# Optimization experiments

Hardware: AMD Instinct MI355X
Metric: run time of the kernel (lower is better)

Reference implementation:

```python
import jax, jax.numpy as jnp
import numpy as np

B, S, D = 4, 2048, 768
H = 12
DH = D // H
NUM_WAY = 4
DFF = 4 * D  # FFN expansion scale=4
EPS = 1e-6


def setup_inputs() -> dict:
    key = jax.random.key(0)
    ks = jax.random.split(key, 20)
    s = 0.02
    inp = {
        "x": jax.random.normal(ks[0], (B, S, D), jnp.float32),
        "w": jax.random.randint(ks[1], (B, S), 0, NUM_WAY, jnp.int64),
        # LayerNorm 1
        "ln1_g": jnp.ones((D,), jnp.float32),
        "ln1_b": jnp.zeros((D,), jnp.float32),
        # Multi-head attention projections (input_dim=out_dim=D)
        "wq": jax.random.normal(ks[2], (D, D), jnp.float32) * s,
        "bq": jnp.zeros((D,), jnp.float32),
        "wk": jax.random.normal(ks[3], (D, D), jnp.float32) * s,
        "bk": jnp.zeros((D,), jnp.float32),
        "wv": jax.random.normal(ks[4], (D, D), jnp.float32) * s,
        "bv": jnp.zeros((D,), jnp.float32),
        "wo": jax.random.normal(ks[5], (D, D), jnp.float32) * s,
        "bo": jnp.zeros((D,), jnp.float32),
        # Way classifier
        "wcls": jax.random.normal(ks[6], (D, NUM_WAY), jnp.float32) * s,
        "bcls": jnp.zeros((NUM_WAY,), jnp.float32),
        # num_way stacked FFN experts: Linear(D,4D) -> ReLU -> Linear(4D,D)
        "w1": jax.random.normal(ks[7], (NUM_WAY, D, DFF), jnp.float32) * s,
        "b1": jnp.zeros((NUM_WAY, DFF), jnp.float32),
        "w2": jax.random.normal(ks[8], (NUM_WAY, DFF, D), jnp.float32) * s,
        "b2": jnp.zeros((NUM_WAY, D), jnp.float32),
    }
    return inp


def _layernorm(x, g, b):
    mu = jnp.mean(x, axis=-1, keepdims=True)
    var = jnp.mean(jnp.square(x - mu), axis=-1, keepdims=True)
    return (x - mu) * jax.lax.rsqrt(var + EPS) * g + b


def reference(x, w, ln1_g, ln1_b, wq, bq, wk, bk, wv, bv, wo, bo,
              wcls, bcls, w1, b1, w2, b2):
    # pre-LN
    xn = _layernorm(x, ln1_g, ln1_b)
    # multi-head self-attention (q = k = v = xn)
    q = (xn @ wq + bq).reshape(B, S, H, DH)
    k = (xn @ wk + bk).reshape(B, S, H, DH)
    v = (xn @ wv + bv).reshape(B, S, H, DH)
    scores = jnp.einsum('bqhd,bkhd->bhqk', q, k) / jnp.sqrt(jnp.float32(DH))
    attn = jax.nn.softmax(scores, axis=-1)
    ctx = jnp.einsum('bhqk,bkhd->bqhd', attn, v).reshape(B, S, D)
    ctx = ctx @ wo + bo
    # dropout is identity at inference; residual
    out = ctx + x
    # dense compute-all-experts FFN, then per-token select by routing id w
    # (mask-overwrite in original == one-hot select since masks partition)
    ffn_out = jnp.zeros_like(out)
    for ci in range(NUM_WAY):
        h = jax.nn.relu(out @ w1[ci] + b1[ci])        # [B,S,4D]
        fi = h @ w2[ci] + b2[ci]                      # [B,S,D]
        mask = (w == ci).astype(out.dtype)[..., None]  # [B,S,1]
        if ci == 0:
            # original initializes ffn_out with way-0 output everywhere;
            # later ways overwrite where w == ci, net = select expert w
            ffn_out = fi
        else:
            ffn_out = ffn_out * (1.0 - mask) + fi * mask
    way_logits = out @ wcls + bcls  # [B,S,NUM_WAY]
    return ffn_out, way_logits
```

## Files before the change

### kernel.cpp

```cpp
#include <hip/hip_runtime.h>
#include <cstdint>

typedef unsigned short u16;
typedef float f32x4 __attribute__((ext_vector_type(4)));
typedef __bf16 bf16x8 __attribute__((ext_vector_type(8)));

#define LOG2E 1.44269504088896340736f

__device__ __forceinline__ u16 f2bf(float f) {
    union { float f; unsigned u; } v; v.f = f;
    unsigned r = v.u + 0x7fffu + ((v.u >> 16) & 1u);
    return (u16)(r >> 16);
}

__device__ __forceinline__ unsigned cvt_pk_bf16(float lo, float hi) {
    unsigned r;
    asm("v_cvt_pk_bf16_f32 %0, %1, %2" : "=v"(r) : "v"(lo), "v"(hi));
    return r;
}

__device__ __forceinline__ f32x4 mfma16(bf16x8 a, bf16x8 b, f32x4 c) {
    return __builtin_amdgcn_mfma_f32_16x16x32_bf16(a, b, c, 0, 0, 0);
}

__device__ __forceinline__ void gload_lds16(const void* g, void* l) {
    __builtin_amdgcn_global_load_lds(
        (__attribute__((address_space(1))) unsigned int*)(g),
        (__attribute__((address_space(3))) unsigned int*)(l),
        16, 0, 0);
}

#define MB_TOK 8192
#define DM 768
#define HH 12
#define DHD 64
#define NWAY 4
#define DFF 3072
#define SEQ 2048
#define NBATCH 4

__global__ __launch_bounds__(256) void ln_kernel(
    const float* __restrict__ x, const float* __restrict__ g,
    const float* __restrict__ bb, u16* __restrict__ xn)
{
    int row = blockIdx.x, t = threadIdx.x;
    const float* xr = x + (size_t)row * DM;
    float v0 = xr[t], v1 = xr[t + 256], v2 = xr[t + 512];
    float s = v0 + v1 + v2;
    __shared__ float red[4];
    #pragma unroll
    for (int k = 1; k < 64; k <<= 1) s += __shfl_xor(s, k);
    if ((t & 63) == 0) red[t >> 6] = s;
    __syncthreads();
    float mu = (red[0] + red[1] + red[2] + red[3]) * (1.f / 768.f);
    float d0 = v0 - mu, d1 = v1 - mu, d2 = v2 - mu;
    float q = d0 * d0 + d1 * d1 + d2 * d2;
    #pragma unroll
    for (int k = 1; k < 64; k <<= 1) q += __shfl_xor(q, k);
    __syncthreads();
    if ((t & 63) == 0) red[t >> 6] = q;
    __syncthreads();
    float var = (red[0] + red[1] + red[2] + red[3]) * (1.f / 768.f);
    float rs = rsqrtf(var + 1e-6f);
    u16* xo = xn + (size_t)row * DM;
    xo[t]       = f2bf(d0 * rs * g[t]       + bb[t]);
    xo[t + 256] = f2bf(d1 * rs * g[t + 256] + bb[t + 256]);
    xo[t + 512] = f2bf(d2 * rs * g[t + 512] + bb[t + 512]);
}

__global__ __launch_bounds__(256) void transpose_bf16(
    const float* __restrict__ src, u16* __restrict__ dst, int K, int N)
{
    __shared__ float tl[32][33];
    size_t bofs = (size_t)blockIdx.z * K * N;
    src += bofs; dst += bofs;
    int n0 = blockIdx.x * 32, k0 = blockIdx.y * 32;
    int tx = threadIdx.x, ty = threadIdx.y;
    #pragma unroll
    for (int j = 0; j < 4; ++j)
        tl[ty + j * 8][tx] = src[(size_t)(k0 + ty + j * 8) * N + n0 + tx];
    __syncthreads();
    #pragma unroll
    for (int j = 0; j < 4; ++j)
        dst[(size_t)(n0 + ty + j * 8) * K + k0 + tx] = f2bf(tl[tx][ty + j * 8]);
}

__global__ __launch_bounds__(256) void vT_kernel(
    const u16* __restrict__ qkv, u16* __restrict__ vT)
{
    __shared__ u16 tl[32][33];
    int bh = blockIdx.z;
    int b = bh / HH, h = bh % HH;
    int key0 = blockIdx.x * 32;
    int d0 = blockIdx.y * 32;
    int tx = threadIdx.x, ty = threadIdx.y;
    const u16* src = qkv + ((size_t)b * SEQ + key0) * 2304 + 1536 + h * 64 + d0;
    #pragma unroll
    for (int j = 0; j < 4; ++j)
        tl[ty + j * 8][tx] = src[(size_t)(ty + j * 8) * 2304 + tx];
    __syncthreads();
    u16* dst = vT + ((size_t)bh * 64 + d0) * SEQ + key0;
    #pragma unroll
    for (int j = 0; j < 4; ++j)
        dst[(size_t)(ty + j * 8) * SEQ + tx] = tl[tx][ty + j * 8];
}

__global__ void concat_bias_kernel(const float* bq, const float* bk,
                                   const float* bv, float* bqkv)
{
    int i = blockIdx.x * 256 + threadIdx.x;
    if (i < 2304) bqkv[i] = i < 768 ? bq[i] : (i < 1536 ? bk[i - 768] : bv[i - 1536]);
}

__global__ void route_kernel(const int* __restrict__ wl,
                             int* __restrict__ perm, int* __restrict__ eoff,
                             int4* __restrict__ fmap)
{
    __shared__ int cnt[4], cur[4], off[5];
    int tid = threadIdx.x;
    if (tid < 4) cnt[tid] = 0;
    __syncthreads();
    for (int t = tid; t < MB_TOK; t += 256) atomicAdd(&cnt[wl[t] & 3], 1);
    __syncthreads();
    if (tid == 0) {
        off[0] = 0;
        for (int e = 0; e < 4; ++e) off[e + 1] = off[e] + cnt[e];
        int idx = 0;
        for (int e = 0; e < 4; ++e)
            for (int s = 0; s < cnt[e]; s += 128)
                fmap[idx++] = make_int4(e, off[e], s, cnt[e] - s);
        for (; idx < 68; ++idx) fmap[idx] = make_int4(-1, 0, 0, 0);
        for (int e = 0; e < 5; ++e) eoff[e] = off[e];
        for (int e = 0; e < 4; ++e) cur[e] = off[e];
    }
    __syncthreads();
    for (int t = tid; t < MB_TOK; t += 256) {
        int e = wl[t] & 3;
        int pos = atomicAdd(&cur[e], 1);
        perm[pos] = t;
    }
}

template<int MODE, bool RELU, bool RES, bool ST32, bool ST16>
__global__ __launch_bounds__(256, 2) void gemm_bt_kernel(
    const u16* __restrict__ A, const u16* __restrict__ Bt,
    const float* __restrict__ bias, const float* __restrict__ res,
    float* __restrict__ out32, u16* __restrict__ out16,
    int M, int N, int K, int ntn,
    const int* __restrict__ perm, const int4* __restrict__ fmap)
{
    __shared__ __attribute__((aligned(16))) u16 As[128 * 32];
    __shared__ __attribute__((aligned(16))) u16 Bs[128 * 32];
    int tid = threadIdx.x;
    int wv = tid >> 6, ln = tid & 63;
    int bt = blockIdx.x / ntn;
    int tn = (blockIdx.x % ntn) * 128;

    int seg = 0, ms = 0, mb = 128, tm = 0;
    if (MODE != 0) {
        int4 ent = fmap[bt];
        if (ent.x < 0) return;
        seg = ent.y; ms = ent.z; mb = ent.w; if (mb > 128) mb = 128;
        Bt += (size_t)ent.x * N * K;
        bias += ent.x * N;
    } else {
        tm = bt * 128;
    }

    f32x4 acc[4][4];
    #pragma unroll
    for (int i = 0; i < 4; ++i)
        #pragma unroll
        for (int j = 0; j < 4; ++j) acc[i][j] = f32x4{0.f, 0.f, 0.f, 0.f};

    int wr = wv >> 1, wc = wv & 1;
    int lr = ln & 15, hi = ln >> 4;
    int nk = K / 32;

    for (int kk = 0; kk < nk; ++kk) {
        int k0 = kk * 32;
        #pragma unroll
        for (int i = 0; i < 2; ++i) {
            int r = (wv * 2 + i) * 16 + (ln >> 2);
            int am = r < mb ? r : (mb - 1);
            size_t arow;
            if (MODE == 1)      arow = (size_t)perm[seg + ms + am];
            else if (MODE == 2) arow = (size_t)(seg + ms + am);
            else                arow = (size_t)(tm + r);
            gload_lds16(A + arow * K + k0 + (ln & 3) * 8, &As[(wv * 2 + i) * 512]);
        }
        #pragma unroll
        for (int i = 0; i < 2; ++i) {
            int r = (wv * 2 + i) * 16 + (ln >> 2);
            gload_lds16(Bt + (size_t)(tn + r) * K + k0 + (ln & 3) * 8,
                        &Bs[(wv * 2 + i) * 512]);
        }
        __syncthreads();
        bf16x8 a[4], b[4];
        #pragma unroll
        for (int m = 0; m < 4; ++m)
            a[m] = *(const bf16x8*)&As[(wr * 64 + m * 16 + lr) * 32 + hi * 8];
        #pragma unroll
        for (int n = 0; n < 4; ++n)
            b[n] = *(const bf16x8*)&Bs[(wc * 64 + n * 16 + lr) * 32 + hi * 8];
        #pragma unroll
        for (int m = 0; m < 4; ++m)
            #pragma unroll
            for (int n = 0; n < 4; ++n)
                acc[m][n] = mfma16(a[m], b[n], acc[m][n]);
        __syncthreads();
    }

    #pragma unroll
    for (int m = 0; m < 4; ++m) {
        int rb = wr * 64 + m * 16 + hi * 4;
        #pragma unroll
        for (int n = 0; n < 4; ++n) {
            int gcol = tn + wc * 64 + n * 16 + lr;
            float bvv = bias[gcol];
            #pragma unroll
            for (int i = 0; i < 4; ++i) {
                int rml = rb + i;
                float v = acc[m][n][i] + bvv;
                if (RELU) v = v > 0.f ? v : 0.f;
                if (MODE == 0) {
                    size_t grow = (size_t)(tm + rml);
                    if (RES) v += res[grow * N + gcol];
                    if (ST32) out32[grow * N + gcol] = v;
                    if (ST16) out16[grow * N + gcol] = f2bf(v);
                } else {
                    if (rml < mb) {
                        size_t orow = (MODE == 1) ? (size_t)(seg + ms + rml)
                                                  : (size_t)perm[seg + ms + rml];
                        if (ST32) out32[orow * N + gcol] = v;
                        if (ST16) out16[orow * N + gcol] = f2bf(v);
                    }
                }
            }
        }
    }
}

__global__ __launch_bounds__(256, 4) void attn_kernel(
    const u16* __restrict__ qkv, const u16* __restrict__ vT,
    u16* __restrict__ ctx)
{
    __shared__ __attribute__((aligned(16))) u16 Ks[64 * 64];
    __shared__ __attribute__((aligned(16))) u16 Vs[64 * 64];
    int tid = threadIdx.x;
    int wv = tid >> 6, ln = tid & 63;
    int lr = ln & 15, hi = ln >> 4;
    int bh = blockIdx.y;
    int b = bh / HH, h = bh % HH;
    int q0 = blockIdx.x * 64 + wv * 16;
    size_t qrow = (size_t)(b * SEQ + q0 + lr);
    const float C = 0.125f * LOG2E;

    bf16x8 qf[2];
    {
        const u16* qp = qkv + qrow * 2304 + h * 64 + hi * 8;
        qf[0] = *(const bf16x8*)qp;
        qf[1] = *(const bf16x8*)(qp + 32);
    }
    f32x4 o[4];
    #pragma unroll
    for (int i = 0; i < 4; ++i) o[i] = f32x4{0.f, 0.f, 0.f, 0.f};
    float m_run = -INFINITY, l_run = 0.f;

    const size_t kbase = (size_t)b * SEQ * 2304 + 768 + h * 64;
    const u16* vtb = vT + (size_t)bh * 64 * SEQ;
    int scol = (ln & 7) * 8;

    for (int kt = 0; kt < SEQ / 64; ++kt) {
        int key0 = kt * 64;
        #pragma unroll
        for (int i = 0; i < 2; ++i) {
            int r = wv * 16 + i * 8 + (ln >> 3);
            int csrc = scol ^ ((r & 7) * 8);
            gload_lds16(qkv + kbase + (size_t)(key0 + r) * 2304 + csrc,
                        &Ks[(wv * 2 + i) * 512]);
            gload_lds16(vtb + (size_t)r * SEQ + key0 + csrc,
                        &Vs[(wv * 2 + i) * 512]);
        }
        __syncthreads();

        f32x4 sf[4];
        #pragma unroll
        for (int f = 0; f < 4; ++f) {
            int key = f * 16 + lr;
            int sw = (key & 7) * 8;
            bf16x8 klo = *(const bf16x8*)&Ks[key * 64 + ((hi * 8) ^ sw)];
            bf16x8 khi = *(const bf16x8*)&Ks[key * 64 + ((32 + hi * 8) ^ sw)];
            f32x4 s = f32x4{0.f, 0.f, 0.f, 0.f};
            s = mfma16(klo, qf[0], s);
            s = mfma16(khi, qf[1], s);
            sf[f] = s;
        }

        float tmax = sf[0][0];
        #pragma unroll
        for (int f = 0; f < 4; ++f)
            #pragma unroll
            for (int i = 0; i < 4; ++i) tmax = fmaxf(tmax, sf[f][i]);
        tmax = fmaxf(tmax, __shfl_xor(tmax, 16));
        tmax = fmaxf(tmax, __shfl_xor(tmax, 32));

        if (!__all(tmax - m_run <= 64.f)) {
            float m_new = fmaxf(m_run, tmax);
            float corr = exp2f((m_run - m_new) * C);
            l_run *= corr;
            #pragma unroll
            for (int dg = 0; dg < 4; ++dg) {
                o[dg][0] *= corr; o[dg][1] *= corr;
                o[dg][2] *= corr; o[dg][3] *= corr;
            }
            m_run = m_new;
        }

        float c2 = -m_run * C;
        float p[4][4];
        float psum = 0.f;
        #pragma unroll
        for (int f = 0; f < 4; ++f)
            #pragma unroll
            for (int i = 0; i < 4; ++i) {
                p[f][i] = exp2f(fmaf(sf[f][i], C, c2));
                psum += p[f][i];
            }
        psum += __shfl_xor(psum, 16);
        psum += __shfl_xor(psum, 32);
        l_run += psum;

        #pragma unroll
        for (int kf = 0; kf < 2; ++kf) {
            union { bf16x8 v; unsigned u[4]; } pb;
            pb.u[0] = cvt_pk_bf16(p[2 * kf][0], p[2 * kf][1]);
            pb.u[1] = cvt_pk_bf16(p[2 * kf][2], p[2 * kf][3]);
            pb.u[2] = cvt_pk_bf16(p[2 * kf + 1][0], p[2 * kf + 1][1]);
            pb.u[3] = cvt_pk_bf16(p[2 * kf + 1][2], p[2 * kf + 1][3]);
            #pragma unroll
            for (int dg = 0; dg < 4; ++dg) {
                int d = dg * 16 + lr;
                int sw = (d & 7) * 16;
                const char* vb = (const char*)Vs + d * 128;
                union { bf16x8 v; uint2 u[2]; } va;
                va.u[0] = *(const uint2*)(const void*)(vb + ((kf * 64 + hi * 8) ^ sw));
                va.u[1] = *(const uint2*)(const void*)(vb + ((kf * 64 + hi * 8 + 32) ^ sw));
                o[dg] = mfma16(va.v, pb.v, o[dg]);
            }
        }
        __syncthreads();
    }

    float inv = 1.f / l_run;
    #pragma unroll
    for (int dg = 0; dg < 4; ++dg) {
        uint2 pk;
        pk.x = cvt_pk_bf16(o[dg][0] * inv, o[dg][1] * inv);
        pk.y = cvt_pk_bf16(o[dg][2] * inv, o[dg][3] * inv);
        *(uint2*)(void*)&ctx[qrow * DM + h * 64 + dg * 16 + hi * 4] = pk;
    }
}

__global__ __launch_bounds__(256) void cls_kernel(
    const float* __restrict__ outm, const float* __restrict__ wcls,
    const float* __restrict__ bcls, float* __restrict__ dst)
{
    int row = blockIdx.x, t = threadIdx.x;
    const float* xr = outm + (size_t)row * DM;
    float a0 = 0, a1 = 0, a2 = 0, a3 = 0;
    for (int j = t; j < DM; j += 256) {
        float xv = xr[j];
        float4 wv4 = *(const float4*)(const void*)(wcls + (size_t)j * 4);
        a0 += xv * wv4.x; a1 += xv * wv4.y; a2 += xv * wv4.z; a3 += xv * wv4.w;
    }
    #pragma unroll
    for (int k = 1; k < 64; k <<= 1) {
        a0 += __shfl_xor(a0, k); a1 += __shfl_xor(a1, k);
        a2 += __shfl_xor(a2, k); a3 += __shfl_xor(a3, k);
    }
    __shared__ float red[4][4];
    if ((t & 63) == 0) {
        int wid = t >> 6;
        red[wid][0] = a0; red[wid][1] = a1; red[wid][2] = a2; red[wid][3] = a3;
    }
    __syncthreads();
    if (t < 4)
        dst[(size_t)row * 4 + t] =
            red[0][t] + red[1][t] + red[2][t] + red[3][t] + bcls[t];
}

extern "C" void kernel_launch(void* const* d_in, const int* in_sizes, int n_in,
                              void* d_out, int out_size, void* d_ws, size_t ws_size,
                              hipStream_t stream) {
    const float* x      = (const float*)d_in[0];
    const int*   wl     = (const int*)d_in[1];
    const float* ln_g   = (const float*)d_in[2];
    const float* ln_b   = (const float*)d_in[3];
    const float* wq     = (const float*)d_in[4];
    const float* bq     = (const float*)d_in[5];
    const float* wk     = (const float*)d_in[6];
    const float* bk     = (const float*)d_in[7];
    const float* wvv    = (const float*)d_in[8];
    const float* bv     = (const float*)d_in[9];
    const float* wo     = (const float*)d_in[10];
    const float* bo     = (const float*)d_in[11];
    const float* wcls   = (const float*)d_in[12];
    const float* bcls   = (const float*)d_in[13];
    const float* w1     = (const float*)d_in[14];
    const float* b1     = (const float*)d_in[15];
    const float* w2     = (const float*)d_in[16];
    const float* b2     = (const float*)d_in[17];
    float* out = (float*)d_out;

    char* ws = (char*)d_ws;
    u16*   xn    = (u16*)  (ws + 0);
    u16*   qkv   = (u16*)  (ws + 12582912);
    u16*   hbuf  = (u16*)  (ws + 0);
    u16*   ctx   = (u16*)  (ws + 50331648);
    u16*   outb  = (u16*)  (ws + 62914560);
    u16*   wqkvt = (u16*)  (ws + 75497472);
    u16*   wot   = (u16*)  (ws + 79036416);
    u16*   w1t   = (u16*)  (ws + 80216064);
    u16*   w2t   = (u16*)  (ws + 99090432);
    float* bqkv  = (float*)(ws + 117964800);
    int*   perm  = (int*)  (ws + 117974016);
    int*   eoff  = (int*)  (ws + 118006784);
    int4*  fmap  = (int4*) (ws + 118006816);
    u16*   vT    = (u16*)  (ws + 118008064);
    float* outf  = out;

    route_kernel<<<1, 256, 0, stream>>>(wl, perm, eoff, fmap);
    concat_bias_kernel<<<9, 256, 0, stream>>>(bq, bk, bv, bqkv);
    dim3 tb(32, 8);
    transpose_bf16<<<dim3(24, 24, 1), tb, 0, stream>>>(wq,  wqkvt,             768, 768);
    transpose_bf16<<<dim3(24, 24, 1), tb, 0, stream>>>(wk,  wqkvt + 768 * 768, 768, 768);
    transpose_bf16<<<dim3(24, 24, 1), tb, 0, stream>>>(wvv, wqkvt + 2 * 768 * 768, 768, 768);
    transpose_bf16<<<dim3(24, 24, 1), tb, 0, stream>>>(wo,  wot, 768, 768);
    transpose_bf16<<<dim3(96, 24, 4), tb, 0, stream>>>(w1,  w1t, 768, 3072);
    transpose_bf16<<<dim3(24, 96, 4), tb, 0, stream>>>(w2,  w2t, 3072, 768);
    ln_kernel<<<MB_TOK, 256, 0, stream>>>(x, ln_g, ln_b, xn);

    gemm_bt_kernel<0, false, false, false, true><<<64 * 18, 256, 0, stream>>>(
        xn, wqkvt, bqkv, nullptr, nullptr, qkv, MB_TOK, 2304, 768, 18, nullptr, nullptr);

    vT_kernel<<<dim3(64, 2, 48), tb, 0, stream>>>(qkv, vT);

    attn_kernel<<<dim3(32, 48), 256, 0, stream>>>(qkv, vT, ctx);

    gemm_bt_kernel<0, false, true, true, true><<<64 * 6, 256, 0, stream>>>(
        ctx, wot, bo, x, outf, outb, MB_TOK, 768, 768, 6, nullptr, nullptr);

    cls_kernel<<<MB_TOK, 256, 0, stream>>>(outf, wcls, bcls, out + (size_t)MB_TOK * DM);

    gemm_bt_kernel<1, true, false, false, true><<<68 * 24, 256, 0, stream>>>(
        outb, w1t, b1, nullptr, nullptr, hbuf, MB_TOK, DFF, 768, 24, perm, fmap);

    gemm_bt_kernel<2, false, false, true, false><<<68 * 6, 256, 0, stream>>>(
        hbuf, w2t, b2, nullptr, out, nullptr, MB_TOK, 768, DFF, 6, perm, fmap);
}
```

Measured before the change: 410.5 us.

## Restructure attention to 32x32 MFMA tiles with double-buffered K/V and LDS-staged output

The attention kernel now gives each wave 32 query rows using 32x32x16 bf16 MFMAs instead of 16x16x32, so each block covers 128 queries. K/V tiles are double-buffered in LDS so the next tile's loads overlap the current tile's compute, which removes one barrier per iteration. exp2 is mapped directly to the hardware v_exp_f32, P fragments are rearranged with a cross-half lane shuffle, and the output is staged through LDS for coalesced 16-byte stores. The grid is flattened and remapped across heads and batches. The cost is more registers per thread and doubled LDS, which may lower occupancy.

```diff
diff --git a/kernel.cpp b/kernel.cpp
--- a/kernel.cpp
+++ b/kernel.cpp
@@ -3,6 +3,7 @@
 
 typedef unsigned short u16;
 typedef float f32x4 __attribute__((ext_vector_type(4)));
+typedef float f32x16 __attribute__((ext_vector_type(16)));
 typedef __bf16 bf16x8 __attribute__((ext_vector_type(8)));
 
 #define LOG2E 1.44269504088896340736f
@@ -19,8 +20,18 @@
     return r;
 }
 
+__device__ __forceinline__ float exp2_hw(float x) {
+    float r;
+    asm("v_exp_f32 %0, %1" : "=v"(r) : "v"(x));
+    return r;
+}
+
 __device__ __forceinline__ f32x4 mfma16(bf16x8 a, bf16x8 b, f32x4 c) {
     return __builtin_amdgcn_mfma_f32_16x16x32_bf16(a, b, c, 0, 0, 0);
+}
+
+__device__ __forceinline__ f32x16 mfma32(bf16x8 a, bf16x8 b, f32x16 c) {
+    return __builtin_amdgcn_mfma_f32_32x32x16_bf16(a, b, c, 0, 0, 0);
 }
 
 __device__ __forceinline__ void gload_lds16(const void* g, void* l) {
@@ -245,120 +256,140 @@
     const u16* __restrict__ qkv, const u16* __restrict__ vT,
     u16* __restrict__ ctx)
 {
-    __shared__ __attribute__((aligned(16))) u16 Ks[64 * 64];
-    __shared__ __attribute__((aligned(16))) u16 Vs[64 * 64];
+    __shared__ __attribute__((aligned(16))) u16 Ks[2][4096];
+    __shared__ __attribute__((aligned(16))) u16 Vs[2][4096];
     int tid = threadIdx.x;
     int wv = tid >> 6, ln = tid & 63;
-    int lr = ln & 15, hi = ln >> 4;
-    int bh = blockIdx.y;
+    int qv = ln & 31, hi = ln >> 5;
+    int bid = blockIdx.x;
+    int bh = (bid & 7) * 6 + ((bid >> 3) % 6);
+    int qt = (bid >> 3) / 6;
     int b = bh / HH, h = bh % HH;
-    int q0 = blockIdx.x * 64 + wv * 16;
-    size_t qrow = (size_t)(b * SEQ + q0 + lr);
+    int q0 = qt * 128 + wv * 32;
+    size_t qrowb = (size_t)(b * SEQ + q0);
     const float C = 0.125f * LOG2E;
 
-    bf16x8 qf[2];
+    bf16x8 qf[4];
     {
-        const u16* qp = qkv + qrow * 2304 + h * 64 + hi * 8;
-        qf[0] = *(const bf16x8*)qp;
-        qf[1] = *(const bf16x8*)(qp + 32);
-    }
-    f32x4 o[4];
-    #pragma unroll
-    for (int i = 0; i < 4; ++i) o[i] = f32x4{0.f, 0.f, 0.f, 0.f};
-    float m_run = -INFINITY, l_run = 0.f;
-
+        const u16* qp = qkv + (qrowb + qv) * 2304 + h * 64 + hi * 8;
+        #pragma unroll
+        for (int ds = 0; ds < 4; ++ds) qf[ds] = *(const bf16x8*)(qp + ds * 16);
+    }
+
+    int csrc = 8 * ((ln & 7) ^ (ln >> 3));
     const size_t kbase = (size_t)b * SEQ * 2304 + 768 + h * 64;
     const u16* vtb = vT + (size_t)bh * 64 * SEQ;
-    int scol = (ln & 7) * 8;
+    const u16* kp0 = qkv + kbase + (size_t)(wv * 16 + (ln >> 3)) * 2304 + csrc;
+    const u16* kp1 = kp0 + (size_t)8 * 2304;
+    const u16* vp0 = vtb + (size_t)(wv * 16 + (ln >> 3)) * SEQ + csrc;
+    const u16* vp1 = vp0 + (size_t)8 * SEQ;
+
+#define ATTN_STAGE(bf_, t_) do {                                          \
+    gload_lds16(kp0 + (size_t)(t_) * 64 * 2304, &Ks[bf_][(wv * 2) * 512]);\
+    gload_lds16(kp1 + (size_t)(t_) * 64 * 2304, &Ks[bf_][(wv * 2 + 1) * 512]);\
+    gload_lds16(vp0 + (size_t)(t_) * 64, &Vs[bf_][(wv * 2) * 512]);       \
+    gload_lds16(vp1 + (size_t)(t_) * 64, &Vs[bf_][(wv * 2 + 1) * 512]);   \
+} while (0)
+
+    f32x16 oacc[2];
+    #pragma unroll
+    for (int i = 0; i < 2; ++i)
+        #pragma unroll
+        for (int r = 0; r < 16; ++r) oacc[i][r] = 0.f;
+    float m_run = -INFINITY, l_run = 0.f;
+    int ksw = (qv & 7) * 8;
+
+    ATTN_STAGE(0, 0);
 
     for (int kt = 0; kt < SEQ / 64; ++kt) {
-        int key0 = kt * 64;
-        #pragma unroll
-        for (int i = 0; i < 2; ++i) {
-            int r = wv * 16 + i * 8 + (ln >> 3);
-            int csrc = scol ^ ((r & 7) * 8);
-            gload_lds16(qkv + kbase + (size_t)(key0 + r) * 2304 + csrc,
-                        &Ks[(wv * 2 + i) * 512]);
-            gload_lds16(vtb + (size_t)r * SEQ + key0 + csrc,
-                        &Vs[(wv * 2 + i) * 512]);
-        }
+        int bf = kt & 1;
         __syncthreads();
-
-        f32x4 sf[4];
-        #pragma unroll
-        for (int f = 0; f < 4; ++f) {
-            int key = f * 16 + lr;
-            int sw = (key & 7) * 8;
-            bf16x8 klo = *(const bf16x8*)&Ks[key * 64 + ((hi * 8) ^ sw)];
-            bf16x8 khi = *(const bf16x8*)&Ks[key * 64 + ((32 + hi * 8) ^ sw)];
-            f32x4 s = f32x4{0.f, 0.f, 0.f, 0.f};
-            s = mfma16(klo, qf[0], s);
-            s = mfma16(khi, qf[1], s);
-            sf[f] = s;
-        }
-
-        float tmax = sf[0][0];
-        #pragma unroll
-        for (int f = 0; f < 4; ++f)
-            #pragma unroll
-            for (int i = 0; i < 4; ++i) tmax = fmaxf(tmax, sf[f][i]);
-        tmax = fmaxf(tmax, __shfl_xor(tmax, 16));
+        if (kt + 1 < SEQ / 64) ATTN_STAGE(bf ^ 1, kt + 1);
+
+        f32x16 s0, s1;
+        #pragma unroll
+        for (int r = 0; r < 16; ++r) { s0[r] = 0.f; s1[r] = 0.f; }
+        #pragma unroll
+        for (int ds = 0; ds < 4; ++ds) {
+            bf16x8 ka0 = *(const bf16x8*)&Ks[bf][qv * 64 + ((ds * 16 + hi * 8) ^ ksw)];
+            bf16x8 ka1 = *(const bf16x8*)&Ks[bf][(32 + qv) * 64 + ((ds * 16 + hi * 8) ^ ksw)];
+            s0 = mfma32(ka0, qf[ds], s0);
+            s1 = mfma32(ka1, qf[ds], s1);
+        }
+
+        float tmax = s0[0];
+        #pragma unroll
+        for (int r = 1; r < 16; ++r) tmax = fmaxf(tmax, s0[r]);
+        #pragma unroll
+        for (int r = 0; r < 16; ++r) tmax = fmaxf(tmax, s1[r]);
         tmax = fmaxf(tmax, __shfl_xor(tmax, 32));
 
         if (!__all(tmax - m_run <= 64.f)) {
             float m_new = fmaxf(m_run, tmax);
-            float corr = exp2f((m_run - m_new) * C);
+            float corr = exp2_hw((m_run - m_new) * C);
             l_run *= corr;
             #pragma unroll
-            for (int dg = 0; dg < 4; ++dg) {
-                o[dg][0] *= corr; o[dg][1] *= corr;
-                o[dg][2] *= corr; o[dg][3] *= corr;
+            for (int i = 0; i < 2; ++i)
+                #pragma unroll
+                for (int r = 0; r < 16; ++r) oacc[i][r] *= corr;
+            m_run = m_new;
+        }
+        float c2 = -m_run * C;
+        float psum = 0.f;
+        #pragma unroll
+        for (int r = 0; r < 16; ++r) {
+            s0[r] = exp2_hw(fmaf(s0[r], C, c2)); psum += s0[r];
+            s1[r] = exp2_hw(fmaf(s1[r], C, c2)); psum += s1[r];
+        }
+        l_run += psum;
+
+        #pragma unroll
+        for (int kb = 0; kb < 2; ++kb) {
+            #pragma unroll
+            for (int hc = 0; hc < 2; ++hc) {
+                const f32x16& sv = kb ? s1 : s0;
+                unsigned x0 = cvt_pk_bf16(sv[8 * hc + 0], sv[8 * hc + 1]);
+                unsigned x1 = cvt_pk_bf16(sv[8 * hc + 2], sv[8 * hc + 3]);
+                unsigned x2 = cvt_pk_bf16(sv[8 * hc + 4], sv[8 * hc + 5]);
+                unsigned x3 = cvt_pk_bf16(sv[8 * hc + 6], sv[8 * hc + 7]);
+                unsigned t0 = hi ? x0 : x2, t1 = hi ? x1 : x3;
+                unsigned r0 = (unsigned)__shfl_xor((int)t0, 32);
+                unsigned r1 = (unsigned)__shfl_xor((int)t1, 32);
+                union { bf16x8 v; unsigned u[4]; } pf;
+                pf.u[0] = hi ? r0 : x0; pf.u[1] = hi ? r1 : x1;
+                pf.u[2] = hi ? x2 : r0; pf.u[3] = hi ? x3 : r1;
+                int kc = (kb * 32 + hc * 16 + hi * 8) ^ ksw;
+                #pragma unroll
+                for (int dblk = 0; dblk < 2; ++dblk) {
+                    bf16x8 va = *(const bf16x8*)&Vs[bf][(dblk * 32 + qv) * 64 + kc];
+                    oacc[dblk] = mfma32(va, pf.v, oacc[dblk]);
+                }
             }
-            m_run = m_new;
-        }
-
-        float c2 = -m_run * C;
-        float p[4][4];
-        float psum = 0.f;
-        #pragma unroll
-        for (int f = 0; f < 4; ++f)
-            #pragma unroll
-            for (int i = 0; i < 4; ++i) {
-                p[f][i] = exp2f(fmaf(sf[f][i], C, c2));
-                psum += p[f][i];
-            }
-        psum += __shfl_xor(psum, 16);
-        psum += __shfl_xor(psum, 32);
-        l_run += psum;
-
-        #pragma unroll
-        for (int kf = 0; kf < 2; ++kf) {
-            union { bf16x8 v; unsigned u[4]; } pb;
-            pb.u[0] = cvt_pk_bf16(p[2 * kf][0], p[2 * kf][1]);
-            pb.u[1] = cvt_pk_bf16(p[2 * kf][2], p[2 * kf][3]);
-            pb.u[2] = cvt_pk_bf16(p[2 * kf + 1][0], p[2 * kf + 1][1]);
-            pb.u[3] = cvt_pk_bf16(p[2 * kf + 1][2], p[2 * kf + 1][3]);
-            #pragma unroll
-            for (int dg = 0; dg < 4; ++dg) {
-                int d = dg * 16 + lr;
-                int sw = (d & 7) * 16;
-                const char* vb = (const char*)Vs + d * 128;
-                union { bf16x8 v; uint2 u[2]; } va;
-                va.u[0] = *(const uint2*)(const void*)(vb + ((kf * 64 + hi * 8) ^ sw));
-                va.u[1] = *(const uint2*)(const void*)(vb + ((kf * 64 + hi * 8 + 32) ^ sw));
-                o[dg] = mfma16(va.v, pb.v, o[dg]);
-            }
-        }
-        __syncthreads();
-    }
-
-    float inv = 1.f / l_run;
-    #pragma unroll
-    for (int dg = 0; dg < 4; ++dg) {
-        uint2 pk;
-        pk.x = cvt_pk_bf16(o[dg][0] * inv, o[dg][1] * inv);
-        pk.y = cvt_pk_bf16(o[dg][2] * inv, o[dg][3] * inv);
-        *(uint2*)(void*)&ctx[qrow * DM + h * 64 + dg * 16 + hi * 4] = pk;
+        }
+    }
+#undef ATTN_STAGE
+
+    float l_tot = l_run + __shfl_xor(l_run, 32);
+    float inv = 1.f / l_tot;
+
+    __syncthreads();
+    u16* eb = &Ks[0][0] + wv * 2048;
+    #pragma unroll
+    for (int dblk = 0; dblk < 2; ++dblk)
+        #pragma unroll
+        for (int r = 0; r < 16; r += 2) {
+            int d = dblk * 32 + (r & 3) + 8 * (r >> 2) + 4 * hi;
+            unsigned pk = cvt_pk_bf16(oacc[dblk][r] * inv, oacc[dblk][r + 1] * inv);
+            *(unsigned*)&eb[qv * 64 + (d ^ ((qv & 7) * 8))] = pk;
+        }
+    __syncthreads();
+    {
+        u16* ctr = ctx + (qrowb + qv) * DM + h * 64 + hi * 32;
+        #pragma unroll
+        for (int g = 0; g < 4; ++g) {
+            bf16x8 vv = *(const bf16x8*)&eb[qv * 64 + ((hi * 32 + g * 8) ^ ((qv & 7) * 8))];
+            *(bf16x8*)(ctr + g * 8) = vv;
+        }
     }
 }
 
@@ -446,7 +477,7 @@
 
     vT_kernel<<<dim3(64, 2, 48), tb, 0, stream>>>(qkv, vT);
 
-    attn_kernel<<<dim3(32, 48), 256, 0, stream>>>(qkv, vT, ctx);
+    attn_kernel<<<768, 256, 0, stream>>>(qkv, vT, ctx);
 
     gemm_bt_kernel<0, false, true, true, true><<<64 * 6, 256, 0, stream>>>(
         ctx, wot, bo, x, outf, outb, MB_TOK, 768, 768, 6, nullptr, nullptr);
```

Measured after the change: 376.5 us. 1.09x faster.
